# Kernel tuning notes

Measured on AMD Instinct MI355X. Metric: run time of the kernel, lower is better.

Reference implementation:

```python
import jax, jax.numpy as jnp
import numpy as np

BATCH = 4096
IN_DIM = 512
OUT_DIM = 512
GRID_SIZE = 5
K = 3


def _extended_grid():
    # Original: grid = linspace(-1, 1, grid_size+1), spacing h = 2/grid_size.
    # The de Boor-Cox recursion in the source indexes up to grid[grid_size+2k],
    # so we extend the uniform grid to the right with the same spacing.
    h = 2.0 / GRID_SIZE
    return (-1.0 + h * jnp.arange(GRID_SIZE + 2 * K + 1)).astype(jnp.float32)


def bspline_basis(x, grid, k):
    """Vectorized de Boor-Cox recursion.
    x: [..., ] floats; returns basis [..., grid_size + k].
    Identical math to the recursive b_spline_basis in the source, but computed
    bottom-up over all knot intervals at once (no redundant recomputation).
    """
    xe = x[..., None]  # [..., 1]
    # degree-0: indicator of half-open knot intervals, [..., n_knots-1]
    B = ((grid[:-1] <= xe) & (xe < grid[1:])).astype(x.dtype)
    for d in range(1, k + 1):
        n = grid.shape[0] - d - 1
        gi, gid = grid[:n], grid[d:d + n]          # grid[i], grid[i+d]
        gi1, gid1 = grid[1:n + 1], grid[d + 1:d + n + 1]  # grid[i+1], grid[i+d+1]
        # uniform grid -> denominators are d*h, never zero
        B = (xe - gi) / (gid - gi) * B[..., :n] + (gid1 - xe) / (gid1 - gi1) * B[..., 1:n + 1]
    return B  # [..., grid_size + k]


def setup_inputs() -> dict:
    key = jax.random.key(0)
    k1, k2 = jax.random.split(key)
    x = jax.random.uniform(k1, (BATCH, IN_DIM), jnp.float32) * 2.0 - 1.0  # in [-1, 1)
    spline_coeff = jax.random.normal(k2, (IN_DIM, OUT_DIM, GRID_SIZE + K), jnp.float32)
    spline_scaling = jnp.ones((IN_DIM, OUT_DIM), jnp.float32)
    return {"x": x, "spline_coeff": spline_coeff, "spline_scaling": spline_scaling}


def reference(x, spline_coeff, spline_scaling):
    grid = _extended_grid()
    basis = bspline_basis(x, grid, K)  # [B, in_dim, grid_size+k]
    # out[b, j] = sum_i scaling[i,j] * sum_g basis[b,i,g] * coeff[i,j,g]
    return jnp.einsum('big,ijg,ij->bj', basis, spline_coeff, spline_scaling)
```

## Files before the change

### kernel.cpp

```cpp
#include <hip/hip_runtime.h>
#include <hip/hip_bf16.h>
#include <stdint.h>


#define BATCH   4096
#define IN_DIM  512
#define OUT_DIM 512
#define KDIM    (IN_DIM * 8)

typedef short short8 __attribute__((ext_vector_type(8)));
typedef float f32x4  __attribute__((ext_vector_type(4)));

__device__ __forceinline__ unsigned short f2bf(float f) {
  union { float f; unsigned int u; } v; v.f = f;
  unsigned int r = v.u + 0x7FFFu + ((v.u >> 16) & 1u);
  return (unsigned short)(r >> 16);
}

__device__ __forceinline__ void bspline_win(float xv, float* w, int* mm) {
  float t = (xv + 1.0f) * 2.5f;
  int m = (int)t;
  m = m < 0 ? 0 : (m > 4 ? 4 : m);
  float u  = t - (float)m;
  float u2 = u * u, u3 = u2 * u, om = 1.0f - u;
  w[0] = om * om * om * (1.0f / 6.0f);
  w[1] = (3.0f * u3 - 6.0f * u2 + 4.0f) * (1.0f / 6.0f);
  w[2] = (-3.0f * u3 + 3.0f * u2 + 3.0f * u + 1.0f) * (1.0f / 6.0f);
  w[3] = u3 * (1.0f / 6.0f);
  *mm = m;
}

__device__ __forceinline__ short8 basis_pack8(float xv) {
  float w[4]; int m;
  bspline_win(xv, w, &m);
  short8 h = {};
#pragma unroll
  for (int g = 0; g < 8; ++g) {
    int d = g - m + 3;
    float v = (d == 0) ? w[0] : (d == 1) ? w[1] : (d == 2) ? w[2] : (d == 3) ? w[3] : 0.0f;
    h[g] = (short)f2bf(v);
  }
  return h;
}

__device__ __forceinline__ void async_load16(const void* g, void* l) {
  __builtin_amdgcn_global_load_lds(
      (__attribute__((address_space(1))) void*)(uintptr_t)g,
      (__attribute__((address_space(3))) void*)(unsigned int)(uintptr_t)l,
      16, 0, 0);
}


__global__ void kan_basis(const float* __restrict__ x, unsigned short* __restrict__ Ag) {
  int idx = blockIdx.x * 256 + threadIdx.x;
  short8 h = basis_pack8(x[idx]);
  *reinterpret_cast<short8*>(Ag + (size_t)idx * 8) = h;
}

__global__ void kan_pack(const float* __restrict__ coeff, const float* __restrict__ scaling,
                         unsigned short* __restrict__ Wt) {
  int idx = blockIdx.x * 256 + threadIdx.x;
  int i = idx >> 9, j = idx & 511;
  float s = scaling[idx];
  const float4* cp = reinterpret_cast<const float4*>(coeff) + (size_t)idx * 2;
  float4 c0 = cp[0], c1 = cp[1];
  short8 h;
  h[0] = (short)f2bf(c0.x * s); h[1] = (short)f2bf(c0.y * s);
  h[2] = (short)f2bf(c0.z * s); h[3] = (short)f2bf(c0.w * s);
  h[4] = (short)f2bf(c1.x * s); h[5] = (short)f2bf(c1.y * s);
  h[6] = (short)f2bf(c1.z * s); h[7] = (short)f2bf(c1.w * s);
  *reinterpret_cast<short8*>(Wt + (size_t)j * KDIM + i * 8) = h;
}

template <bool USE_WS>
__global__ __launch_bounds__(256, 2)
void kan_gemm(const float* __restrict__ x, const float* __restrict__ coeff,
              const float* __restrict__ scaling,
              const unsigned short* __restrict__ Ag,
              const unsigned short* __restrict__ Wt,
              float* __restrict__ out) {
  __shared__ unsigned short As[64 * 64];
  __shared__ unsigned short Bs[64 * 64];

  const int tid  = threadIdx.x;
  const int lane = tid & 63;
  const int wid  = tid >> 6;
  const int wm = wid >> 1, wn = wid & 1;
  const int ln = lane & 15, quad = lane >> 4;
  const int row0 = blockIdx.y * 64;
  const int col0 = blockIdx.x * 64;

  f32x4 acc[2][2] = {};

  const int lr = lane >> 3;
  const int cg = (lane & 7) ^ lr;

  for (int kt = 0; kt < KDIM / 64; ++kt) {
    const int k0 = kt * 64;
    if constexpr (USE_WS) {
#pragma unroll
      for (int t = 0; t < 2; ++t) {
        const int rbase = wid * 16 + t * 8;
        const unsigned short* ga = Ag + (size_t)(row0 + rbase + lr) * KDIM + k0 + cg * 8;
        async_load16(ga, &As[rbase * 64]);
        const unsigned short* gb = Wt + (size_t)(col0 + rbase + lr) * KDIM + k0 + cg * 8;
        async_load16(gb, &Bs[rbase * 64]);
      }
    } else {
#pragma unroll
      for (int pp = 0; pp < 2; ++pp) {
        const int p  = tid + pp * 256;
        const int rn = p & 63;
        const int il = p >> 6;
        const int sw = ((il ^ (rn & 7)) * 8);
        short8 ha = basis_pack8(x[(size_t)(row0 + rn) * IN_DIM + kt * 8 + il]);
        *reinterpret_cast<short8*>(&As[rn * 64 + sw]) = ha;
        const float* cbase = coeff + (size_t)(kt * 8 + il) * 4096 + (size_t)(col0 + rn) * 8;
        float4 c0 = reinterpret_cast<const float4*>(cbase)[0];
        float4 c1 = reinterpret_cast<const float4*>(cbase)[1];
        float s = scaling[(size_t)(kt * 8 + il) * OUT_DIM + col0 + rn];
        short8 hb;
        hb[0] = (short)f2bf(c0.x * s); hb[1] = (short)f2bf(c0.y * s);
        hb[2] = (short)f2bf(c0.z * s); hb[3] = (short)f2bf(c0.w * s);
        hb[4] = (short)f2bf(c1.x * s); hb[5] = (short)f2bf(c1.y * s);
        hb[6] = (short)f2bf(c1.z * s); hb[7] = (short)f2bf(c1.w * s);
        *reinterpret_cast<short8*>(&Bs[rn * 64 + sw]) = hb;
      }
    }
    __syncthreads();

#pragma unroll
    for (int kk = 0; kk < 2; ++kk) {
      short8 af[2], bfr[2];
#pragma unroll
      for (int mt = 0; mt < 2; ++mt) {
        const int r  = wm * 32 + mt * 16 + ln;
        const int pc = (kk * 4 + quad) ^ (r & 7);
        af[mt] = *reinterpret_cast<const short8*>(&As[r * 64 + pc * 8]);
      }
#pragma unroll
      for (int nt = 0; nt < 2; ++nt) {
        const int c  = wn * 32 + nt * 16 + ln;
        const int pc = (kk * 4 + quad) ^ (c & 7);
        bfr[nt] = *reinterpret_cast<const short8*>(&Bs[c * 64 + pc * 8]);
      }
#pragma unroll
      for (int mt = 0; mt < 2; ++mt)
#pragma unroll
        for (int nt = 0; nt < 2; ++nt)
          acc[mt][nt] = __builtin_amdgcn_mfma_f32_16x16x32_bf16(af[mt], bfr[nt], acc[mt][nt], 0, 0, 0);
    }
    __syncthreads();
  }

#pragma unroll
  for (int mt = 0; mt < 2; ++mt)
#pragma unroll
    for (int nt = 0; nt < 2; ++nt) {
      const int col = col0 + wn * 32 + nt * 16 + ln;
#pragma unroll
      for (int r = 0; r < 4; ++r) {
        const int row = row0 + wm * 32 + mt * 16 + quad * 4 + r;
        out[(size_t)row * OUT_DIM + col] = acc[mt][nt][r];
      }
    }
}

extern "C" void kernel_launch(void* const* d_in, const int* in_sizes, int n_in,
                              void* d_out, int out_size, void* d_ws, size_t ws_size,
                              hipStream_t stream) {
  const float* x       = (const float*)d_in[0];
  const float* coeff   = (const float*)d_in[1];
  const float* scaling = (const float*)d_in[2];
  float* out = (float*)d_out;

  const size_t needA = (size_t)BATCH * KDIM * 2;
  const size_t needW = (size_t)OUT_DIM * KDIM * 2;

  if (ws_size >= needA + needW) {
    unsigned short* Ag = (unsigned short*)d_ws;
    unsigned short* Wt = (unsigned short*)((char*)d_ws + needA);
    kan_basis<<<(BATCH * IN_DIM) / 256, 256, 0, stream>>>(x, Ag);
    kan_pack<<<(IN_DIM * OUT_DIM) / 256, 256, 0, stream>>>(coeff, scaling, Wt);
    kan_gemm<true><<<dim3(OUT_DIM / 64, BATCH / 64), 256, 0, stream>>>(
        x, coeff, scaling, Ag, Wt, out);
  } else {
    kan_gemm<false><<<dim3(OUT_DIM / 64, BATCH / 64), 256, 0, stream>>>(
        x, coeff, scaling, nullptr, nullptr, out);
  }
}
```

Before: 119.7 us.

## Split GEMM along K with atomic accumulation and merge prep kernels

```diff
diff --git a/kernel.cpp b/kernel.cpp
--- a/kernel.cpp
+++ b/kernel.cpp
@@ -7,6 +7,8 @@
 #define IN_DIM  512
 #define OUT_DIM 512
 #define KDIM    (IN_DIM * 8)
+#define KSPLIT  4
+#define KT_PER_SPLIT (KDIM / 64 / KSPLIT)
 
 typedef short short8 __attribute__((ext_vector_type(8)));
 typedef float f32x4  __attribute__((ext_vector_type(4)));
@@ -50,35 +52,35 @@
       16, 0, 0);
 }
 
-
-__global__ void kan_basis(const float* __restrict__ x, unsigned short* __restrict__ Ag) {
-  int idx = blockIdx.x * 256 + threadIdx.x;
-  short8 h = basis_pack8(x[idx]);
-  *reinterpret_cast<short8*>(Ag + (size_t)idx * 8) = h;
-}
-
-__global__ void kan_pack(const float* __restrict__ coeff, const float* __restrict__ scaling,
+__global__ void kan_prep(const float* __restrict__ x,
+                         const float* __restrict__ coeff,
+                         const float* __restrict__ scaling,
+                         unsigned short* __restrict__ Ag,
                          unsigned short* __restrict__ Wt) {
-  int idx = blockIdx.x * 256 + threadIdx.x;
-  int i = idx >> 9, j = idx & 511;
-  float s = scaling[idx];
-  const float4* cp = reinterpret_cast<const float4*>(coeff) + (size_t)idx * 2;
-  float4 c0 = cp[0], c1 = cp[1];
-  short8 h;
-  h[0] = (short)f2bf(c0.x * s); h[1] = (short)f2bf(c0.y * s);
-  h[2] = (short)f2bf(c0.z * s); h[3] = (short)f2bf(c0.w * s);
-  h[4] = (short)f2bf(c1.x * s); h[5] = (short)f2bf(c1.y * s);
-  h[6] = (short)f2bf(c1.z * s); h[7] = (short)f2bf(c1.w * s);
-  *reinterpret_cast<short8*>(Wt + (size_t)j * KDIM + i * 8) = h;
-}
-
-template <bool USE_WS>
-__global__ __launch_bounds__(256, 2)
-void kan_gemm(const float* __restrict__ x, const float* __restrict__ coeff,
-              const float* __restrict__ scaling,
-              const unsigned short* __restrict__ Ag,
-              const unsigned short* __restrict__ Wt,
-              float* __restrict__ out) {
+  const int b = blockIdx.x;
+  if (b < (BATCH * IN_DIM) / 256) {
+    int idx = b * 256 + threadIdx.x;
+    short8 h = basis_pack8(x[idx]);
+    *reinterpret_cast<short8*>(Ag + (size_t)idx * 8) = h;
+  } else {
+    int idx = (b - (BATCH * IN_DIM) / 256) * 256 + threadIdx.x;
+    int i = idx >> 9, j = idx & 511;
+    float s = scaling[idx];
+    const float4* cp = reinterpret_cast<const float4*>(coeff) + (size_t)idx * 2;
+    float4 c0 = cp[0], c1 = cp[1];
+    short8 h;
+    h[0] = (short)f2bf(c0.x * s); h[1] = (short)f2bf(c0.y * s);
+    h[2] = (short)f2bf(c0.z * s); h[3] = (short)f2bf(c0.w * s);
+    h[4] = (short)f2bf(c1.x * s); h[5] = (short)f2bf(c1.y * s);
+    h[6] = (short)f2bf(c1.z * s); h[7] = (short)f2bf(c1.w * s);
+    *reinterpret_cast<short8*>(Wt + (size_t)j * KDIM + i * 8) = h;
+  }
+}
+
+__global__ __launch_bounds__(256, 4)
+void kan_gemm_sk(const unsigned short* __restrict__ Ag,
+                 const unsigned short* __restrict__ Wt,
+                 float* __restrict__ out) {
   __shared__ unsigned short As[64 * 64];
   __shared__ unsigned short Bs[64 * 64];
 
@@ -89,43 +91,22 @@
   const int ln = lane & 15, quad = lane >> 4;
   const int row0 = blockIdx.y * 64;
   const int col0 = blockIdx.x * 64;
+  const int kt0  = blockIdx.z * KT_PER_SPLIT;
 
   f32x4 acc[2][2] = {};
 
   const int lr = lane >> 3;
   const int cg = (lane & 7) ^ lr;
 
-  for (int kt = 0; kt < KDIM / 64; ++kt) {
+  for (int kt = kt0; kt < kt0 + KT_PER_SPLIT; ++kt) {
     const int k0 = kt * 64;
-    if constexpr (USE_WS) {
-#pragma unroll
-      for (int t = 0; t < 2; ++t) {
-        const int rbase = wid * 16 + t * 8;
-        const unsigned short* ga = Ag + (size_t)(row0 + rbase + lr) * KDIM + k0 + cg * 8;
-        async_load16(ga, &As[rbase * 64]);
-        const unsigned short* gb = Wt + (size_t)(col0 + rbase + lr) * KDIM + k0 + cg * 8;
-        async_load16(gb, &Bs[rbase * 64]);
-      }
-    } else {
-#pragma unroll
-      for (int pp = 0; pp < 2; ++pp) {
-        const int p  = tid + pp * 256;
-        const int rn = p & 63;
-        const int il = p >> 6;
-        const int sw = ((il ^ (rn & 7)) * 8);
-        short8 ha = basis_pack8(x[(size_t)(row0 + rn) * IN_DIM + kt * 8 + il]);
-        *reinterpret_cast<short8*>(&As[rn * 64 + sw]) = ha;
-        const float* cbase = coeff + (size_t)(kt * 8 + il) * 4096 + (size_t)(col0 + rn) * 8;
-        float4 c0 = reinterpret_cast<const float4*>(cbase)[0];
-        float4 c1 = reinterpret_cast<const float4*>(cbase)[1];
-        float s = scaling[(size_t)(kt * 8 + il) * OUT_DIM + col0 + rn];
-        short8 hb;
-        hb[0] = (short)f2bf(c0.x * s); hb[1] = (short)f2bf(c0.y * s);
-        hb[2] = (short)f2bf(c0.z * s); hb[3] = (short)f2bf(c0.w * s);
-        hb[4] = (short)f2bf(c1.x * s); hb[5] = (short)f2bf(c1.y * s);
-        hb[6] = (short)f2bf(c1.z * s); hb[7] = (short)f2bf(c1.w * s);
-        *reinterpret_cast<short8*>(&Bs[rn * 64 + sw]) = hb;
-      }
+#pragma unroll
+    for (int t = 0; t < 2; ++t) {
+      const int rbase = wid * 16 + t * 8;
+      const unsigned short* ga = Ag + (size_t)(row0 + rbase + lr) * KDIM + k0 + cg * 8;
+      async_load16(ga, &As[rbase * 64]);
+      const unsigned short* gb = Wt + (size_t)(col0 + rbase + lr) * KDIM + k0 + cg * 8;
+      async_load16(gb, &Bs[rbase * 64]);
     }
     __syncthreads();
 
@@ -153,6 +134,79 @@
     __syncthreads();
   }
 
+#pragma unroll
+  for (int mt = 0; mt < 2; ++mt)
+#pragma unroll
+    for (int nt = 0; nt < 2; ++nt) {
+      const int col = col0 + wn * 32 + nt * 16 + ln;
+#pragma unroll
+      for (int r = 0; r < 4; ++r) {
+        const int row = row0 + wm * 32 + mt * 16 + quad * 4 + r;
+        unsafeAtomicAdd(&out[(size_t)row * OUT_DIM + col], acc[mt][nt][r]);
+      }
+    }
+}
+
+__global__ __launch_bounds__(256, 2)
+void kan_gemm_fb(const float* __restrict__ x, const float* __restrict__ coeff,
+                 const float* __restrict__ scaling, float* __restrict__ out) {
+  __shared__ unsigned short As[64 * 64];
+  __shared__ unsigned short Bs[64 * 64];
+
+  const int tid  = threadIdx.x;
+  const int lane = tid & 63;
+  const int wid  = tid >> 6;
+  const int wm = wid >> 1, wn = wid & 1;
+  const int ln = lane & 15, quad = lane >> 4;
+  const int row0 = blockIdx.y * 64;
+  const int col0 = blockIdx.x * 64;
+
+  f32x4 acc[2][2] = {};
+
+  for (int kt = 0; kt < KDIM / 64; ++kt) {
+#pragma unroll
+    for (int pp = 0; pp < 2; ++pp) {
+      const int p  = tid + pp * 256;
+      const int rn = p & 63;
+      const int il = p >> 6;
+      const int sw = ((il ^ (rn & 7)) * 8);
+      short8 ha = basis_pack8(x[(size_t)(row0 + rn) * IN_DIM + kt * 8 + il]);
+      *reinterpret_cast<short8*>(&As[rn * 64 + sw]) = ha;
+      const float* cbase = coeff + (size_t)(kt * 8 + il) * 4096 + (size_t)(col0 + rn) * 8;
+      float4 c0 = reinterpret_cast<const float4*>(cbase)[0];
+      float4 c1 = reinterpret_cast<const float4*>(cbase)[1];
+      float s = scaling[(size_t)(kt * 8 + il) * OUT_DIM + col0 + rn];
+      short8 hb;
+      hb[0] = (short)f2bf(c0.x * s); hb[1] = (short)f2bf(c0.y * s);
+      hb[2] = (short)f2bf(c0.z * s); hb[3] = (short)f2bf(c0.w * s);
+      hb[4] = (short)f2bf(c1.x * s); hb[5] = (short)f2bf(c1.y * s);
+      hb[6] = (short)f2bf(c1.z * s); hb[7] = (short)f2bf(c1.w * s);
+      *reinterpret_cast<short8*>(&Bs[rn * 64 + sw]) = hb;
+    }
+    __syncthreads();
+#pragma unroll
+    for (int kk = 0; kk < 2; ++kk) {
+      short8 af[2], bfr[2];
+#pragma unroll
+      for (int mt = 0; mt < 2; ++mt) {
+        const int r  = wm * 32 + mt * 16 + ln;
+        const int pc = (kk * 4 + quad) ^ (r & 7);
+        af[mt] = *reinterpret_cast<const short8*>(&As[r * 64 + pc * 8]);
+      }
+#pragma unroll
+      for (int nt = 0; nt < 2; ++nt) {
+        const int c  = wn * 32 + nt * 16 + ln;
+        const int pc = (kk * 4 + quad) ^ (c & 7);
+        bfr[nt] = *reinterpret_cast<const short8*>(&Bs[c * 64 + pc * 8]);
+      }
+#pragma unroll
+      for (int mt = 0; mt < 2; ++mt)
+#pragma unroll
+        for (int nt = 0; nt < 2; ++nt)
+          acc[mt][nt] = __builtin_amdgcn_mfma_f32_16x16x32_bf16(af[mt], bfr[nt], acc[mt][nt], 0, 0, 0);
+    }
+    __syncthreads();
+  }
 #pragma unroll
   for (int mt = 0; mt < 2; ++mt)
 #pragma unroll
@@ -180,12 +234,11 @@
   if (ws_size >= needA + needW) {
     unsigned short* Ag = (unsigned short*)d_ws;
     unsigned short* Wt = (unsigned short*)((char*)d_ws + needA);
-    kan_basis<<<(BATCH * IN_DIM) / 256, 256, 0, stream>>>(x, Ag);
-    kan_pack<<<(IN_DIM * OUT_DIM) / 256, 256, 0, stream>>>(coeff, scaling, Wt);
-    kan_gemm<true><<<dim3(OUT_DIM / 64, BATCH / 64), 256, 0, stream>>>(
-        x, coeff, scaling, Ag, Wt, out);
+    hipMemsetAsync(out, 0, (size_t)out_size * sizeof(float), stream);
+    kan_prep<<<(BATCH * IN_DIM) / 256 + (IN_DIM * OUT_DIM) / 256, 256, 0, stream>>>(
+        x, coeff, scaling, Ag, Wt);
+    kan_gemm_sk<<<dim3(OUT_DIM / 64, BATCH / 64, KSPLIT), 256, 0, stream>>>(Ag, Wt, out);
   } else {
-    kan_gemm<false><<<dim3(OUT_DIM / 64, BATCH / 64), 256, 0, stream>>>(
-        x, coeff, scaling, nullptr, nullptr, out);
-  }
-}
+    kan_gemm_fb<<<dim3(OUT_DIM / 64, BATCH / 64), 256, 0, stream>>>(x, coeff, scaling, out);
+  }
+}
```

Result: slower. 125.7 us (+5.0%).
